# Kernel tuning notes

Measured on AMD Instinct MI355X. Metric: run time of the kernel, lower is better.

The kernel has to match this reference:

```python
import jax, jax.numpy as jnp
import numpy as np

# dims: Q queries, K hops (topk), N relation groups, M padded nodes/group
Q, K, N, M = 64, 2, 32, 64
E, D, R, S = 256, 1024, 200, 8192  # embs_size, model_size, n_rel, seq positions


def setup_inputs() -> dict:
    key = jax.random.key(0)
    ks = jax.random.split(key, 10)
    hidden_states = jax.random.normal(ks[0], (S, D), jnp.float32)
    nodes = jax.random.normal(ks[1], (Q, K, N, M, E), jnp.float32)
    # ragged groups: zero-pad beyond a random valid length (mirrors F.pad + stack)
    lengths = jax.random.randint(ks[2], (Q, K, N), 1, M + 1)
    valid = jnp.arange(M)[None, None, None, :] < lengths[..., None]
    nodes = nodes * valid[..., None]
    prob_idx = jax.random.randint(ks[3], (Q, K, N), 0, R)
    gnn_idx = jnp.arange(Q, dtype=jnp.int32)          # gnn_mask positions
    rel_idx = jnp.arange(Q, dtype=jnp.int32) + Q      # rel_mask positions (disjoint)
    sc = lambda fan: float(1.0 / np.sqrt(fan))
    u = lambda k, shp, fan: jax.random.uniform(k, shp, jnp.float32, -sc(fan), sc(fan))
    Wc = u(ks[4], (D, R), D); bc = jnp.zeros((R,), jnp.float32)
    Wq = u(ks[5], (D, D), D); bq = jnp.zeros((D,), jnp.float32)
    Wn = u(ks[6], (E, D), E); bn = jnp.zeros((D,), jnp.float32)
    Wg = u(ks[7], (E, D), E); bg = jnp.zeros((D,), jnp.float32)
    return {"hidden_states": hidden_states, "nodes": nodes, "prob_idx": prob_idx,
            "gnn_idx": gnn_idx, "rel_idx": rel_idx,
            "Wc": Wc, "bc": bc, "Wq": Wq, "bq": bq,
            "Wn": Wn, "bn": bn, "Wg": Wg, "bg": bg}


def reference(hidden_states, nodes, prob_idx, gnn_idx, rel_idx,
              Wc, bc, Wq, bq, Wn, bn, Wg, bg):
    Qn, Kn, Nn, Mn, En = nodes.shape
    # classification_head: Linear + Softmax over relations
    rel_prob = jax.nn.softmax(hidden_states[rel_idx] @ Wc + bc, axis=1)  # [Q,R]
    # gather per-group relation probabilities (extract_values_from_tensor)
    probs = jnp.take_along_axis(rel_prob, prob_idx.reshape(Qn, Kn * Nn), axis=1)
    probs = probs.reshape(Qn, Kn, Nn)                                     # [Q,K,N]
    # mask from first feature of padded node embeddings (as in calculate_scores)
    mask = nodes[..., 0] != 0                                             # [Q,K,N,M]
    # query_reprj and nodes_reprj (Linear + Tanh)
    gq = jnp.tanh(hidden_states[gnn_idx] @ Wq + bq)                       # [Q,D]
    gn = jnp.tanh(jnp.einsum('qknme,ed->qknmd', nodes, Wn) + bn)          # [Q,K,N,M,D]
    dots = jnp.einsum('qknmd,qd->qknm', gn, gq)                           # [Q,K,N,M]
    attn = jax.nn.softmax(dots, axis=3)            # softmax over nodes within group
    logits = attn * probs[..., None] / 0.1         # scale by group prob / temperature
    # global softmax over all (group, node) slots per (query, hop)
    wa = jax.nn.softmax(logits.reshape(Qn, Kn, Nn * Mn), axis=-1)
    wa = wa.reshape(Qn, Kn, Nn, Mn)
    wa = jnp.where(mask, wa, 0.0)
    # weighted mean over the flattened N*M slots, then mean over topk hops
    mean_emb = jnp.mean(nodes * wa[..., None], axis=(2, 3))               # [Q,K,E]
    pooled = mean_emb.mean(axis=1)                                        # [Q,E]
    out = jnp.tanh(pooled @ Wg + bg)                                      # gnn_reprj
    return hidden_states.at[gnn_idx].add(out)
```

## Files before the change

### kernel.cpp

```cpp
#include <hip/hip_runtime.h>
#include <hip/hip_bf16.h>
#include <math.h>

#define QDIM 64
#define KDIM 2
#define NDIM 32
#define MDIM 64
#define EDIM 256
#define DDIM 1024
#define RDIM 200
#define SDIM 8192
#define GCOUNT (QDIM * KDIM * NDIM)

typedef short short8_t __attribute__((ext_vector_type(8)));
typedef float f32x4 __attribute__((ext_vector_type(4)));

__device__ __forceinline__ float tanh_c(float x) {
    float e = __expf(2.0f * x);
    return 1.0f - 2.0f * __builtin_amdgcn_rcpf(1.0f + e);
}

__device__ __forceinline__ uint32_t f2bf(float f) {
    uint32_t u = __float_as_uint(f);
    return (u + 0x7fffu + ((u >> 16) & 1u)) >> 16;
}
__device__ __forceinline__ float bf2f(unsigned short h) {
    return __uint_as_float(((uint32_t)h) << 16);
}

__global__ __launch_bounds__(256) void prologue_kernel(
    const float* __restrict__ hs, float* __restrict__ out,
    const float* __restrict__ Wn, short* __restrict__ wnpk,
    const int* __restrict__ gnn_idx, const float* __restrict__ Wq,
    const float* __restrict__ bq, float* __restrict__ gqo,
    const int* __restrict__ rel_idx, const float* __restrict__ Wc,
    const float* __restrict__ bc, float* __restrict__ rel_prob,
    const float* __restrict__ nodes, int* __restrict__ nvarr,
    int* __restrict__ bkt) {
    const int b = blockIdx.x, t = threadIdx.x;
    __shared__ float row[DDIM];
    __shared__ float arr[256];

    if (b < 2048) {
        const float4* src = (const float4*)hs;
        float4* dst = (float4*)out;
        int i = b * 256 + t;
#pragma unroll
        for (int r = 0; r < 4; ++r) dst[i + r * 524288] = src[i + r * 524288];
    } else if (b < 2176) {
        int tid = (b - 2048) * 256 + t;
        int lane = tid & 63, ks = (tid >> 6) & 7, ntg = tid >> 9;
        int low = lane & 15, hi = lane >> 4;
        short8_t o;
#pragma unroll
        for (int j = 0; j < 8; ++j) {
            int k = ks * 32 + hi * 8 + j;
            int d = ntg * 16 + low;
            o[j] = (short)f2bf(Wn[(size_t)k * DDIM + d]);
        }
        *(short8_t*)(wnpk + (size_t)tid * 8) = o;
    } else if (b < 2432) {
        int bb = b - 2176;
        int q = bb >> 2, seg = bb & 3;
        const float* src = hs + (size_t)gnn_idx[q] * DDIM;
        for (int i = t; i < DDIM; i += 256) row[i] = src[i];
        __syncthreads();
        int d = seg * 256 + t;
        float a = bq[d];
#pragma unroll 8
        for (int k = 0; k < DDIM; ++k) a += row[k] * Wq[(size_t)k * DDIM + d];
        gqo[(size_t)q * DDIM + d] = tanh_c(a);
    } else if (b < 2496) {
        int q = b - 2432;
        const float* src = hs + (size_t)rel_idx[q] * DDIM;
        for (int i = t; i < DDIM; i += 256) row[i] = src[i];
        __syncthreads();
        float lg = -INFINITY;
        if (t < RDIM) {
            float a = bc[t];
            for (int k = 0; k < DDIM; ++k) a += row[k] * Wc[(size_t)k * RDIM + t];
            lg = a;
        }
        arr[t] = lg;
        __syncthreads();
        for (int s = 128; s > 0; s >>= 1) {
            if (t < s) arr[t] = fmaxf(arr[t], arr[t + s]);
            __syncthreads();
        }
        float mx = arr[0];
        __syncthreads();
        float ex = (t < RDIM) ? __expf(lg - mx) : 0.0f;
        arr[t] = ex;
        __syncthreads();
        for (int s = 128; s > 0; s >>= 1) {
            if (t < s) arr[t] += arr[t + s];
            __syncthreads();
        }
        float sm = arr[0];
        if (t < RDIM) rel_prob[q * RDIM + t] = ex / sm;
    } else {
        int g = (b - 2496) * 4 + (t >> 6);
        int lane = t & 63;
        float f0 = nodes[(size_t)g * (MDIM * EDIM) + (size_t)lane * EDIM];
        unsigned long long mk = __ballot(f0 != 0.0f);
        if (lane == 0) {
            int nv = __popcll(mk);
            nvarr[g] = nv;
            int mt = (nv + 15) >> 4;
            if (mt < 1) mt = 1;
            atomicAdd(&bkt[mt - 1], 1);
        }
    }
}

__global__ __launch_bounds__(256) void scatter_kernel(const int* __restrict__ nvarr,
                                                      int* __restrict__ bkt,
                                                      int* __restrict__ glist) {
    int g = blockIdx.x * 256 + threadIdx.x;
    int nv = nvarr[g];
    int mt = (nv + 15) >> 4;
    if (mt < 1) mt = 1;
    int base = 0;
#pragma unroll
    for (int k = 0; k < 3; ++k)
        if (k < mt - 1) base += bkt[k];
    int pos = base + atomicAdd(&bkt[4 + (mt - 1)], 1);
    glist[pos] = g | (mt << 16);
}

#define WREG 9216

template <int MT>
__device__ __forceinline__ void wave_body(
    char* ldsw, int g, int q, const float* __restrict__ nodes,
    const short* __restrict__ wnpk, const float* __restrict__ bn,
    const float* __restrict__ gq, const float* __restrict__ rel_prob,
    const int* __restrict__ prob_idx, float* __restrict__ gvec,
    float* __restrict__ gden, float* __restrict__ gmx) {
    const int lane = threadIdx.x & 63;
    const int low = lane & 15, hi = lane >> 4;
    constexpr int NS = MT * 16, TAIL = 64 - NS;

    short8_t af[MT][8];
    {
        const float4* src = (const float4*)(nodes + (size_t)g * (MDIM * EDIM));
#pragma unroll
        for (int mt = 0; mt < MT; ++mt) {
#pragma unroll
            for (int i = 0; i < 16; ++i) {
                int idx4 = i * 64 + lane;
                float4 v = src[mt * 1024 + idx4];
                int r = idx4 >> 6, c4 = idx4 & 63;
                int off = (r * 512 + c4 * 8) ^ ((r & 7) << 4);
                uint32_t w0 = f2bf(v.x) | (f2bf(v.y) << 16);
                uint32_t w1 = f2bf(v.z) | (f2bf(v.w) << 16);
                *(uint2*)(ldsw + off) = make_uint2(w0, w1);
            }
            asm volatile("s_waitcnt lgkmcnt(0)" ::: "memory");
#pragma unroll
            for (int ks = 0; ks < 8; ++ks) {
                int off = (low * 512 + ks * 64 + hi * 16) ^ ((low & 7) << 4);
                af[mt][ks] = *(const short8_t*)(ldsw + off);
            }
            asm volatile("s_waitcnt lgkmcnt(0)" ::: "memory");
        }
    }

    float dacc[MT][4];
#pragma unroll
    for (int mt = 0; mt < MT; ++mt)
#pragma unroll
        for (int jj = 0; jj < 4; ++jj) dacc[mt][jj] = 0.f;
    float cpart = 0.f;
    const float* gqrow = gq + (size_t)q * DDIM;
    const short8_t* bb = (const short8_t*)wnpk + lane;
    for (int ntg = 0; ntg < 64; ++ntg) {
        int d = ntg * 16 + low;
        float gqv = gqrow[d];
        float bnv = bn[d];
        cpart += tanh_c(bnv) * gqv;
        f32x4 acc[MT];
#pragma unroll
        for (int mt = 0; mt < MT; ++mt) acc[mt] = (f32x4){0.f, 0.f, 0.f, 0.f};
        const short8_t* bp = bb + (size_t)ntg * 512;
#pragma unroll
        for (int ks = 0; ks < 8; ++ks) {
            short8_t bf = bp[ks * 64];
#pragma unroll
            for (int mt = 0; mt < MT; ++mt)
                acc[mt] = __builtin_amdgcn_mfma_f32_16x16x32_bf16(af[mt][ks], bf, acc[mt], 0, 0, 0);
        }
#pragma unroll
        for (int mt = 0; mt < MT; ++mt)
#pragma unroll
            for (int jj = 0; jj < 4; ++jj)
                dacc[mt][jj] += tanh_c(acc[mt][jj] + bnv) * gqv;
    }

#pragma unroll
    for (int mt = 0; mt < MT; ++mt)
#pragma unroll
        for (int jj = 0; jj < 4; ++jj) {
            float v = dacc[mt][jj];
            v += __shfl_xor(v, 1);
            v += __shfl_xor(v, 2);
            v += __shfl_xor(v, 4);
            v += __shfl_xor(v, 8);
            dacc[mt][jj] = v;
        }
    float cq;
    {
        float cw = cpart;
#pragma unroll
        for (int off = 32; off > 0; off >>= 1) cw += __shfl_xor(cw, off);
        cq = 0.25f * cw;
    }

    float mx = dacc[0][0];
#pragma unroll
    for (int mt = 0; mt < MT; ++mt)
#pragma unroll
        for (int jj = 0; jj < 4; ++jj) mx = fmaxf(mx, dacc[mt][jj]);
    mx = fmaxf(mx, __shfl_xor(mx, 16));
    mx = fmaxf(mx, __shfl_xor(mx, 32));
    if (TAIL > 0) mx = fmaxf(mx, cq);
    float ex[MT][4];
    float sm = 0.f;
#pragma unroll
    for (int mt = 0; mt < MT; ++mt)
#pragma unroll
        for (int jj = 0; jj < 4; ++jj) {
            ex[mt][jj] = __expf(dacc[mt][jj] - mx);
            sm += ex[mt][jj];
        }
    sm += __shfl_xor(sm, 16);
    sm += __shfl_xor(sm, 32);
    float ext = __expf(cq - mx);
    if (TAIL > 0) sm += (float)TAIL * ext;
    float pr = rel_prob[(size_t)q * RDIM + prob_idx[g]];
    float p10 = pr * 10.0f / sm;
#pragma unroll
    for (int mt = 0; mt < MT; ++mt)
#pragma unroll
        for (int jj = 0; jj < 4; ++jj) ex[mt][jj] *= p10;
    float lgvt = ext * p10;
    float gm = ex[0][0];
#pragma unroll
    for (int mt = 0; mt < MT; ++mt)
#pragma unroll
        for (int jj = 0; jj < 4; ++jj) gm = fmaxf(gm, ex[mt][jj]);
    gm = fmaxf(gm, __shfl_xor(gm, 16));
    gm = fmaxf(gm, __shfl_xor(gm, 32));
    if (TAIL > 0) gm = fmaxf(gm, lgvt);
    float el[MT][4];
    float den = 0.f;
#pragma unroll
    for (int mt = 0; mt < MT; ++mt)
#pragma unroll
        for (int jj = 0; jj < 4; ++jj) {
            el[mt][jj] = __expf(ex[mt][jj] - gm);
            den += el[mt][jj];
        }
    den += __shfl_xor(den, 16);
    den += __shfl_xor(den, 32);
    if (TAIL > 0) den += (float)TAIL * __expf(lgvt - gm);
    if (lane == 0) {
        gden[g] = den;
        gmx[g] = gm;
    }

    float* lvarr = (float*)(ldsw + 8192);
    float* mkarr = lvarr + 64;
#pragma unroll
    for (int mt = 0; mt < MT; ++mt)
#pragma unroll
        for (int jj = 0; jj < 4; ++jj) lvarr[mt * 16 + hi * 4 + jj] = el[mt][jj];
    if (hi == 0) {
#pragma unroll
        for (int mt = 0; mt < MT; ++mt) {
            unsigned short s0 = (unsigned short)af[mt][0][0];
            mkarr[mt * 16 + low] = ((s0 & 0x7fffu) != 0) ? 1.0f : 0.0f;
        }
    }
    asm volatile("s_waitcnt lgkmcnt(0)" ::: "memory");
    float lvm[MT];
#pragma unroll
    for (int mt = 0; mt < MT; ++mt) lvm[mt] = lvarr[mt * 16 + low] * mkarr[mt * 16 + low];
    asm volatile("s_waitcnt lgkmcnt(0)" ::: "memory");

    float ac[8][8];
#pragma unroll
    for (int ks = 0; ks < 8; ++ks)
#pragma unroll
        for (int j = 0; j < 8; ++j) ac[ks][j] = 0.f;
#pragma unroll
    for (int mt = 0; mt < MT; ++mt) {
        float lw = lvm[mt];
#pragma unroll
        for (int ks = 0; ks < 8; ++ks)
#pragma unroll
            for (int j = 0; j < 8; ++j)
                ac[ks][j] += bf2f((unsigned short)af[mt][ks][j]) * lw;
    }
#pragma unroll
    for (int ks = 0; ks < 8; ++ks)
#pragma unroll
        for (int j = 0; j < 8; ++j) {
            float a = ac[ks][j];
            a += __shfl_xor(a, 1);
            a += __shfl_xor(a, 2);
            a += __shfl_xor(a, 4);
            a += __shfl_xor(a, 8);
            ac[ks][j] = a;
        }
    float* vb = lvarr;
#pragma unroll
    for (int ks = 0; ks < 8; ++ks)
#pragma unroll
        for (int j = 0; j < 8; ++j) vb[ks * 32 + hi * 8 + j] = ac[ks][j];
    asm volatile("s_waitcnt lgkmcnt(0)" ::: "memory");
    float4 ov = ((const float4*)vb)[lane];
    *(float4*)(gvec + (size_t)g * EDIM + lane * 4) = ov;
}

__global__ __launch_bounds__(256, 2) void phase1_mfma(
    const float* __restrict__ nodes, const short* __restrict__ wnpk,
    const float* __restrict__ bn, const float* __restrict__ gq,
    const float* __restrict__ rel_prob, const int* __restrict__ prob_idx,
    const int* __restrict__ glist, float* __restrict__ gvec,
    float* __restrict__ gden, float* __restrict__ gmx) {
    __shared__ char lds[4 * WREG];
    int w = threadIdx.x >> 6;
    int pk = glist[blockIdx.x * 4 + w];
    int g = pk & 0xFFFF;
    int mt = pk >> 16;
    int q = g >> 6;
    char* ldsw = lds + w * WREG;
    switch (mt) {
        case 1: wave_body<1>(ldsw, g, q, nodes, wnpk, bn, gq, rel_prob, prob_idx, gvec, gden, gmx); break;
        case 2: wave_body<2>(ldsw, g, q, nodes, wnpk, bn, gq, rel_prob, prob_idx, gvec, gden, gmx); break;
        case 3: wave_body<3>(ldsw, g, q, nodes, wnpk, bn, gq, rel_prob, prob_idx, gvec, gden, gmx); break;
        default: wave_body<4>(ldsw, g, q, nodes, wnpk, bn, gq, rel_prob, prob_idx, gvec, gden, gmx); break;
    }
}

__global__ __launch_bounds__(256) void combine_kernel(const float* __restrict__ gvec,
                                                      const float* __restrict__ gden,
                                                      const float* __restrict__ gmx,
                                                      float* __restrict__ memb) {
    int qk = blockIdx.x, t = threadIdx.x;
    __shared__ float sgm[NDIM], sden[NDIM];
    if (t < NDIM) {
        sgm[t] = gmx[qk * NDIM + t];
        sden[t] = gden[qk * NDIM + t];
    }
    __syncthreads();
    float gm = -INFINITY;
    for (int n = 0; n < NDIM; ++n) gm = fmaxf(gm, sgm[n]);
    float gs = 0.f;
    for (int n = 0; n < NDIM; ++n) gs += sden[n] * __expf(sgm[n] - gm);
    float me = 0.f;
    for (int n = 0; n < NDIM; ++n)
        me += gvec[(size_t)(qk * NDIM + n) * EDIM + t] * __expf(sgm[n] - gm);
    memb[(size_t)qk * EDIM + t] = me / (gs * (float)(NDIM * MDIM));
}

__global__ __launch_bounds__(256) void out_kernel(const float* __restrict__ memb,
                                                  const float* __restrict__ Wg,
                                                  const float* __restrict__ bg,
                                                  const int* __restrict__ gnn_idx,
                                                  float* __restrict__ out) {
    int q = blockIdx.x, t = threadIdx.x;
    __shared__ float pooled[EDIM];
    pooled[t] = 0.5f * (memb[(size_t)(q * 2 + 0) * EDIM + t] + memb[(size_t)(q * 2 + 1) * EDIM + t]);
    __syncthreads();
    float4 a = ((const float4*)bg)[t];
    const float4* Wg4 = (const float4*)Wg;
    for (int e = 0; e < EDIM; ++e) {
        float p = pooled[e];
        float4 w = Wg4[(size_t)e * (DDIM / 4) + t];
        a.x += p * w.x; a.y += p * w.y; a.z += p * w.z; a.w += p * w.w;
    }
    float4* op = (float4*)(out + (size_t)gnn_idx[q] * DDIM);
    float4 cur = op[t];
    cur.x += tanh_c(a.x);
    cur.y += tanh_c(a.y);
    cur.z += tanh_c(a.z);
    cur.w += tanh_c(a.w);
    op[t] = cur;
}

extern "C" void kernel_launch(void* const* d_in, const int* in_sizes, int n_in,
                              void* d_out, int out_size, void* d_ws, size_t ws_size,
                              hipStream_t stream) {
    const float* hs = (const float*)d_in[0];
    const float* nodes = (const float*)d_in[1];
    const int* prob_idx = (const int*)d_in[2];
    const int* gnn_idx = (const int*)d_in[3];
    const int* rel_idx = (const int*)d_in[4];
    const float* Wc = (const float*)d_in[5];
    const float* bc = (const float*)d_in[6];
    const float* Wq = (const float*)d_in[7];
    const float* bq = (const float*)d_in[8];
    const float* Wn = (const float*)d_in[9];
    const float* bn = (const float*)d_in[10];
    const float* Wg = (const float*)d_in[11];
    const float* bg = (const float*)d_in[12];
    float* out = (float*)d_out;
    float* ws = (float*)d_ws;

    float* relprob = ws;
    float* gqbuf = ws + 16384;
    float* gvec = gqbuf + (size_t)QDIM * DDIM;
    float* gdenA = gvec + (size_t)GCOUNT * EDIM;
    float* gmaxA = gdenA + GCOUNT;
    float* membuf = gmaxA + GCOUNT;
    short* wnpk = (short*)(membuf + (size_t)QDIM * KDIM * EDIM);
    int* nvarr = (int*)(wnpk + (size_t)EDIM * DDIM);
    int* bkt = nvarr + GCOUNT;
    int* glist = bkt + 8;

    hipMemsetAsync(bkt, 0, 8 * sizeof(int), stream);
    prologue_kernel<<<3520, 256, 0, stream>>>(hs, out, Wn, wnpk, gnn_idx, Wq, bq,
                                              gqbuf, rel_idx, Wc, bc, relprob,
                                              nodes, nvarr, bkt);
    scatter_kernel<<<GCOUNT / 256, 256, 0, stream>>>(nvarr, bkt, glist);
    phase1_mfma<<<GCOUNT / 4, 256, 0, stream>>>(nodes, wnpk, bn, gqbuf, relprob,
                                                prob_idx, glist, gvec, gdenA, gmaxA);
    combine_kernel<<<QDIM * KDIM, 256, 0, stream>>>(gvec, gdenA, gmaxA, membuf);
    out_kernel<<<QDIM, 256, 0, stream>>>(membuf, Wg, bg, gnn_idx, out);
}
```

Baseline: 319.8 us.

## Load node tiles directly into MFMA registers and use one-wave blocks with single-block scatter

Node rows are now read from global memory straight into the MFMA A-fragment layout and converted to bf16 in registers, which removes the LDS staging round-trip and its swizzle. The main kernel switches to one 64-thread block per group with a small shared scratch, so waves are scheduled independently rather than four per block. Bucket counting moves into a single 1024-thread scatter block that uses shared atomics, which drops the global atomics and the memset. The direct loads are narrower per lane and less coalesced than before, and the serial single-block scatter may add latency.

```diff
diff --git a/kernel.cpp b/kernel.cpp
--- a/kernel.cpp
+++ b/kernel.cpp
@@ -35,8 +35,7 @@
     const float* __restrict__ bq, float* __restrict__ gqo,
     const int* __restrict__ rel_idx, const float* __restrict__ Wc,
     const float* __restrict__ bc, float* __restrict__ rel_prob,
-    const float* __restrict__ nodes, int* __restrict__ nvarr,
-    int* __restrict__ bkt) {
+    const float* __restrict__ nodes, int* __restrict__ nvarr) {
     const int b = blockIdx.x, t = threadIdx.x;
     __shared__ float row[DDIM];
     __shared__ float arr[256];
@@ -103,66 +102,72 @@
         int lane = t & 63;
         float f0 = nodes[(size_t)g * (MDIM * EDIM) + (size_t)lane * EDIM];
         unsigned long long mk = __ballot(f0 != 0.0f);
-        if (lane == 0) {
-            int nv = __popcll(mk);
-            nvarr[g] = nv;
-            int mt = (nv + 15) >> 4;
-            if (mt < 1) mt = 1;
-            atomicAdd(&bkt[mt - 1], 1);
-        }
-    }
-}
-
-__global__ __launch_bounds__(256) void scatter_kernel(const int* __restrict__ nvarr,
-                                                      int* __restrict__ bkt,
-                                                      int* __restrict__ glist) {
-    int g = blockIdx.x * 256 + threadIdx.x;
-    int nv = nvarr[g];
-    int mt = (nv + 15) >> 4;
-    if (mt < 1) mt = 1;
-    int base = 0;
-#pragma unroll
-    for (int k = 0; k < 3; ++k)
-        if (k < mt - 1) base += bkt[k];
-    int pos = base + atomicAdd(&bkt[4 + (mt - 1)], 1);
-    glist[pos] = g | (mt << 16);
-}
-
-#define WREG 9216
+        if (lane == 0) nvarr[g] = __popcll(mk);
+    }
+}
+
+__global__ __launch_bounds__(1024) void scatter_kernel(const int* __restrict__ nvarr,
+                                                       int* __restrict__ glist) {
+    __shared__ int cnt[4], base[4], cur[4];
+    int t = threadIdx.x;
+    if (t < 4) cnt[t] = 0;
+    __syncthreads();
+    int mts[4];
+#pragma unroll
+    for (int r = 0; r < 4; ++r) {
+        int g = t + r * 1024;
+        int nv = nvarr[g];
+        int mt = (nv + 15) >> 4;
+        if (mt < 1) mt = 1;
+        mts[r] = mt;
+        atomicAdd(&cnt[mt - 1], 1);
+    }
+    __syncthreads();
+    if (t == 0) {
+        base[3] = 0;
+        base[2] = cnt[3];
+        base[1] = cnt[3] + cnt[2];
+        base[0] = cnt[3] + cnt[2] + cnt[1];
+        cur[0] = cur[1] = cur[2] = cur[3] = 0;
+    }
+    __syncthreads();
+#pragma unroll
+    for (int r = 0; r < 4; ++r) {
+        int g = t + r * 1024;
+        int mt = mts[r];
+        int pos = base[mt - 1] + atomicAdd(&cur[mt - 1], 1);
+        glist[pos] = g | (mt << 16);
+    }
+}
 
 template <int MT>
 __device__ __forceinline__ void wave_body(
-    char* ldsw, int g, int q, const float* __restrict__ nodes,
+    float* scratch, int g, int q, const float* __restrict__ nodes,
     const short* __restrict__ wnpk, const float* __restrict__ bn,
     const float* __restrict__ gq, const float* __restrict__ rel_prob,
     const int* __restrict__ prob_idx, float* __restrict__ gvec,
     float* __restrict__ gden, float* __restrict__ gmx) {
     const int lane = threadIdx.x & 63;
     const int low = lane & 15, hi = lane >> 4;
-    constexpr int NS = MT * 16, TAIL = 64 - NS;
+    constexpr int TAIL = 64 - MT * 16;
 
     short8_t af[MT][8];
     {
-        const float4* src = (const float4*)(nodes + (size_t)g * (MDIM * EDIM));
+        const float* srcA = nodes + (size_t)g * (MDIM * EDIM);
 #pragma unroll
         for (int mt = 0; mt < MT; ++mt) {
-#pragma unroll
-            for (int i = 0; i < 16; ++i) {
-                int idx4 = i * 64 + lane;
-                float4 v = src[mt * 1024 + idx4];
-                int r = idx4 >> 6, c4 = idx4 & 63;
-                int off = (r * 512 + c4 * 8) ^ ((r & 7) << 4);
-                uint32_t w0 = f2bf(v.x) | (f2bf(v.y) << 16);
-                uint32_t w1 = f2bf(v.z) | (f2bf(v.w) << 16);
-                *(uint2*)(ldsw + off) = make_uint2(w0, w1);
+            const float* rowp = srcA + (size_t)(mt * 16 + low) * EDIM + hi * 8;
+#pragma unroll
+            for (int ks = 0; ks < 8; ++ks) {
+                float4 a = *(const float4*)(rowp + ks * 32);
+                float4 b = *(const float4*)(rowp + ks * 32 + 4);
+                short8_t o;
+                o[0] = (short)f2bf(a.x); o[1] = (short)f2bf(a.y);
+                o[2] = (short)f2bf(a.z); o[3] = (short)f2bf(a.w);
+                o[4] = (short)f2bf(b.x); o[5] = (short)f2bf(b.y);
+                o[6] = (short)f2bf(b.z); o[7] = (short)f2bf(b.w);
+                af[mt][ks] = o;
             }
-            asm volatile("s_waitcnt lgkmcnt(0)" ::: "memory");
-#pragma unroll
-            for (int ks = 0; ks < 8; ++ks) {
-                int off = (low * 512 + ks * 64 + hi * 16) ^ ((low & 7) << 4);
-                af[mt][ks] = *(const short8_t*)(ldsw + off);
-            }
-            asm volatile("s_waitcnt lgkmcnt(0)" ::: "memory");
         }
     }
 
@@ -269,8 +274,9 @@
         gmx[g] = gm;
     }
 
-    float* lvarr = (float*)(ldsw + 8192);
-    float* mkarr = lvarr + 64;
+    float* lvarr = scratch;
+    float* mkarr = scratch + 64;
+    float* vb = scratch + 128;
 #pragma unroll
     for (int mt = 0; mt < MT; ++mt)
 #pragma unroll
@@ -286,61 +292,50 @@
     float lvm[MT];
 #pragma unroll
     for (int mt = 0; mt < MT; ++mt) lvm[mt] = lvarr[mt * 16 + low] * mkarr[mt * 16 + low];
-    asm volatile("s_waitcnt lgkmcnt(0)" ::: "memory");
-
-    float ac[8][8];
-#pragma unroll
-    for (int ks = 0; ks < 8; ++ks)
-#pragma unroll
-        for (int j = 0; j < 8; ++j) ac[ks][j] = 0.f;
-#pragma unroll
-    for (int mt = 0; mt < MT; ++mt) {
-        float lw = lvm[mt];
-#pragma unroll
-        for (int ks = 0; ks < 8; ++ks)
+
+#pragma unroll
+    for (int ks = 0; ks < 8; ++ks) {
+        float acj[8];
+#pragma unroll
+        for (int j = 0; j < 8; ++j) acj[j] = 0.f;
+#pragma unroll
+        for (int mt = 0; mt < MT; ++mt) {
+            float lw = lvm[mt];
 #pragma unroll
             for (int j = 0; j < 8; ++j)
-                ac[ks][j] += bf2f((unsigned short)af[mt][ks][j]) * lw;
-    }
-#pragma unroll
-    for (int ks = 0; ks < 8; ++ks)
+                acj[j] += bf2f((unsigned short)af[mt][ks][j]) * lw;
+        }
 #pragma unroll
         for (int j = 0; j < 8; ++j) {
-            float a = ac[ks][j];
+            float a = acj[j];
             a += __shfl_xor(a, 1);
             a += __shfl_xor(a, 2);
             a += __shfl_xor(a, 4);
             a += __shfl_xor(a, 8);
-            ac[ks][j] = a;
-        }
-    float* vb = lvarr;
-#pragma unroll
-    for (int ks = 0; ks < 8; ++ks)
-#pragma unroll
-        for (int j = 0; j < 8; ++j) vb[ks * 32 + hi * 8 + j] = ac[ks][j];
+            if (low == 0) vb[ks * 32 + hi * 8 + j] = a;
+        }
+    }
     asm volatile("s_waitcnt lgkmcnt(0)" ::: "memory");
     float4 ov = ((const float4*)vb)[lane];
     *(float4*)(gvec + (size_t)g * EDIM + lane * 4) = ov;
 }
 
-__global__ __launch_bounds__(256, 2) void phase1_mfma(
+__global__ __launch_bounds__(64, 4) void phase1_mfma(
     const float* __restrict__ nodes, const short* __restrict__ wnpk,
     const float* __restrict__ bn, const float* __restrict__ gq,
     const float* __restrict__ rel_prob, const int* __restrict__ prob_idx,
     const int* __restrict__ glist, float* __restrict__ gvec,
     float* __restrict__ gden, float* __restrict__ gmx) {
-    __shared__ char lds[4 * WREG];
-    int w = threadIdx.x >> 6;
-    int pk = glist[blockIdx.x * 4 + w];
+    __shared__ float scratch[384];
+    int pk = glist[blockIdx.x];
     int g = pk & 0xFFFF;
     int mt = pk >> 16;
     int q = g >> 6;
-    char* ldsw = lds + w * WREG;
     switch (mt) {
-        case 1: wave_body<1>(ldsw, g, q, nodes, wnpk, bn, gq, rel_prob, prob_idx, gvec, gden, gmx); break;
-        case 2: wave_body<2>(ldsw, g, q, nodes, wnpk, bn, gq, rel_prob, prob_idx, gvec, gden, gmx); break;
-        case 3: wave_body<3>(ldsw, g, q, nodes, wnpk, bn, gq, rel_prob, prob_idx, gvec, gden, gmx); break;
-        default: wave_body<4>(ldsw, g, q, nodes, wnpk, bn, gq, rel_prob, prob_idx, gvec, gden, gmx); break;
+        case 1: wave_body<1>(scratch, g, q, nodes, wnpk, bn, gq, rel_prob, prob_idx, gvec, gden, gmx); break;
+        case 2: wave_body<2>(scratch, g, q, nodes, wnpk, bn, gq, rel_prob, prob_idx, gvec, gden, gmx); break;
+        case 3: wave_body<3>(scratch, g, q, nodes, wnpk, bn, gq, rel_prob, prob_idx, gvec, gden, gmx); break;
+        default: wave_body<4>(scratch, g, q, nodes, wnpk, bn, gq, rel_prob, prob_idx, gvec, gden, gmx); break;
     }
 }
 
@@ -417,16 +412,14 @@
     float* membuf = gmaxA + GCOUNT;
     short* wnpk = (short*)(membuf + (size_t)QDIM * KDIM * EDIM);
     int* nvarr = (int*)(wnpk + (size_t)EDIM * DDIM);
-    int* bkt = nvarr + GCOUNT;
-    int* glist = bkt + 8;
-
-    hipMemsetAsync(bkt, 0, 8 * sizeof(int), stream);
+    int* glist = nvarr + GCOUNT;
+
     prologue_kernel<<<3520, 256, 0, stream>>>(hs, out, Wn, wnpk, gnn_idx, Wq, bq,
                                               gqbuf, rel_idx, Wc, bc, relprob,
-                                              nodes, nvarr, bkt);
-    scatter_kernel<<<GCOUNT / 256, 256, 0, stream>>>(nvarr, bkt, glist);
-    phase1_mfma<<<GCOUNT / 4, 256, 0, stream>>>(nodes, wnpk, bn, gqbuf, relprob,
-                                                prob_idx, glist, gvec, gdenA, gmaxA);
+                                              nodes, nvarr);
+    scatter_kernel<<<1, 1024, 0, stream>>>(nvarr, glist);
+    phase1_mfma<<<GCOUNT, 64, 0, stream>>>(nodes, wnpk, bn, gqbuf, relprob,
+                                           prob_idx, glist, gvec, gdenA, gmaxA);
     combine_kernel<<<QDIM * KDIM, 256, 0, stream>>>(gvec, gdenA, gmaxA, membuf);
     out_kernel<<<QDIM, 256, 0, stream>>>(membuf, Wg, bg, gnn_idx, out);
 }
```

Result: slower. 683.3 us (+113.6%).
